# Kernel optimization log

Measured on AMD Instinct MI355X. Metric: run time of the kernel, lower is better.

## Reference

```python
import jax, jax.numpy as jnp
import numpy as np

N, E, G = 200000, 1200000, 2048
NODE_DIM, H = 5, 64
NEG_SLOPE = 0.2


def setup_inputs() -> dict:
    key = jax.random.key(0)
    ks = jax.random.split(key, 20)
    def glorot(k, shape):
        fan = sum(shape) if len(shape) > 1 else shape[0] + 1
        return jax.random.normal(k, shape, jnp.float32) * jnp.sqrt(2.0 / fan)
    inp = {
        'x': jax.random.normal(ks[0], (N, NODE_DIM), jnp.float32),
        'edge_index': jax.random.randint(ks[1], (2, E), 0, N, jnp.int64),
        'batch': jnp.sort(jax.random.randint(ks[2], (N,), 0, G, jnp.int64)),
        'embed_W': glorot(ks[3], (NODE_DIM, H)), 'embed_b': jnp.zeros((H,), jnp.float32),
        'g1_W': glorot(ks[4], (H, H)), 'g1_asrc': glorot(ks[5], (H,)), 'g1_adst': glorot(ks[6], (H,)), 'g1_b': jnp.zeros((H,), jnp.float32),
        'g2_W': glorot(ks[7], (H, H)), 'g2_asrc': glorot(ks[8], (H,)), 'g2_adst': glorot(ks[9], (H,)), 'g2_b': jnp.zeros((H,), jnp.float32),
        'fc1_W': glorot(ks[10], (2 * H, 64)), 'fc1_b': jnp.zeros((64,), jnp.float32),
        'fc2_W': glorot(ks[11], (64, 32)), 'fc2_b': jnp.zeros((32,), jnp.float32),
        'fc3_W': glorot(ks[12], (32, 1)), 'fc3_b': jnp.zeros((1,), jnp.float32),
    }
    return inp


def gat_conv(x, src, dst, W, a_src, a_dst, b):
    # x: [N, H] -> h: [N, H]; edges (with self-loops) src->dst
    h = x @ W
    alpha_s = h @ a_src  # [N]
    alpha_d = h @ a_dst  # [N]
    e = jax.nn.leaky_relu(alpha_s[src] + alpha_d[dst], NEG_SLOPE)  # [E']
    m = jax.ops.segment_max(e, dst, num_segments=N)
    w = jnp.exp(e - m[dst])
    denom = jax.ops.segment_sum(w, dst, num_segments=N)
    alpha = w / (denom[dst] + 1e-16)
    out = jax.ops.segment_sum(h[src] * alpha[:, None], dst, num_segments=N)
    return out + b


def reference(x, edge_index, batch, embed_W, embed_b,
              g1_W, g1_asrc, g1_adst, g1_b,
              g2_W, g2_asrc, g2_adst, g2_b,
              fc1_W, fc1_b, fc2_W, fc2_b, fc3_W, fc3_b):
    # add self loops once (PyG GATConv default add_self_loops=True)
    loops = jnp.arange(N, dtype=edge_index.dtype)
    src = jnp.concatenate([edge_index[0], loops])
    dst = jnp.concatenate([edge_index[1], loops])

    h = x @ embed_W + embed_b
    h = gat_conv(h, src, dst, g1_W, g1_asrc, g1_adst, g1_b)
    h = jax.nn.relu(h)
    h = gat_conv(h, src, dst, g2_W, g2_asrc, g2_adst, g2_b)

    # global mean / max pooling per graph
    cnt = jax.ops.segment_sum(jnp.ones((N,), h.dtype), batch, num_segments=G)
    mean = jax.ops.segment_sum(h, batch, num_segments=G) / jnp.maximum(cnt, 1.0)[:, None]
    mx = jax.ops.segment_max(h, batch, num_segments=G)
    mx = jnp.where(cnt[:, None] > 0, mx, 0.0)
    g = jnp.concatenate([mean, mx], axis=1)  # [G, 2H]

    g = jax.nn.relu(g @ fc1_W + fc1_b)
    g = jax.nn.relu(g @ fc2_W + fc2_b)
    return g @ fc3_W + fc3_b  # [G, 1]
```

## Files before the change

kernel.cpp:

```cpp
#include <hip/hip_runtime.h>
#include <hip/hip_bf16.h>
#include <hip/hip_fp16.h>

#define HD 64
#define NODE_DIM 5
#define NEG_SLOPE 0.2f
#define GT 64
#define BSH 9
#define BNODES 512
#define NBMAX 512
#define BCAP 4096
#define EPB 8
#define LDH 72

typedef _Float16 f16x8 __attribute__((ext_vector_type(8)));
typedef float f32x4 __attribute__((ext_vector_type(4)));

template <bool EMBED>
__global__ __launch_bounds__(256) void gemm_alpha_k(
    const void* __restrict__ hin, const float* __restrict__ embW,
    const float* __restrict__ embB, const float* __restrict__ W,
    const float* __restrict__ asrc, const float* __restrict__ adst,
    __half* __restrict__ hout, float* __restrict__ alpha_s,
    float* __restrict__ alpha_d, int N) {
    __shared__ _Float16 hs[GT * LDH];
    __shared__ _Float16 Wt[HD * LDH];
    __shared__ float xe[GT * NODE_DIM];
    __shared__ float we[NODE_DIM * HD + HD];
    const int t = threadIdx.x;
    const int n0 = blockIdx.x * GT;
    if (n0 >= N) return;
    const int rem = N - n0;

#pragma unroll
    for (int j = 0; j < 16; j++) {
        int idx = t + 256 * j;
        int k = idx >> 6, n = idx & 63;
        Wt[n * LDH + k] = (_Float16)W[idx];
    }

    if (EMBED) {
        const float* xin = (const float*)hin;
        for (int j = t; j < GT * NODE_DIM; j += 256)
            xe[j] = (j < rem * NODE_DIM) ? xin[(size_t)n0 * NODE_DIM + j] : 0.0f;
        for (int j = t; j < NODE_DIM * HD + HD; j += 256)
            we[j] = (j < NODE_DIM * HD) ? embW[j] : embB[j - NODE_DIM * HD];
        __syncthreads();
        int r = t >> 2, d0 = (t & 3) * 16;
#pragma unroll
        for (int jj = 0; jj < 16; jj++) {
            int d = d0 + jj;
            float acc = we[NODE_DIM * HD + d];
#pragma unroll
            for (int k = 0; k < NODE_DIM; k++)
                acc = fmaf(xe[r * NODE_DIM + k], we[k * HD + d], acc);
            hs[r * LDH + d] = (r < rem) ? (_Float16)acc : (_Float16)0.0f;
        }
    } else {
        const short4* g4 = (const short4*)((const __half*)hin + (size_t)n0 * HD);
#pragma unroll
        for (int j = 0; j < 4; j++) {
            int idx = t + 256 * j;
            int row = idx >> 4, c4 = idx & 15;
            short4 v = {0, 0, 0, 0};
            if (row < rem) v = g4[idx];
            *(short4*)(hs + row * LDH + c4 * 4) = v;
        }
    }
    __syncthreads();

    const int lane = t & 63;
    const int w = t >> 6;
    const int r16 = lane & 15;
    const int g = lane >> 4;

    const _Float16* hrow = hs + (w * 16 + r16) * LDH + g * 8;
    f16x8 b0 = *(const f16x8*)(hrow);
    f16x8 b1 = *(const f16x8*)(hrow + 32);

    f32x4 acc[4];
#pragma unroll
    for (int mt = 0; mt < 4; mt++) acc[mt] = (f32x4){0.f, 0.f, 0.f, 0.f};

#pragma unroll
    for (int mt = 0; mt < 4; mt++) {
        const _Float16* arow = Wt + (mt * 16 + r16) * LDH + g * 8;
        f16x8 a0 = *(const f16x8*)(arow);
        f16x8 a1 = *(const f16x8*)(arow + 32);
        acc[mt] = __builtin_amdgcn_mfma_f32_16x16x32_f16(a0, b0, acc[mt], 0, 0, 0);
        acc[mt] = __builtin_amdgcn_mfma_f32_16x16x32_f16(a1, b1, acc[mt], 0, 0, 0);
    }

    const int node = n0 + w * 16 + r16;
    float ps = 0.0f, pd = 0.0f;
    if (node < N) {
#pragma unroll
        for (int mt = 0; mt < 4; mt++) {
            float4 av = ((const float4*)asrc)[mt * 4 + g];
            float4 bv = ((const float4*)adst)[mt * 4 + g];
            ps += acc[mt][0] * av.x + acc[mt][1] * av.y +
                  acc[mt][2] * av.z + acc[mt][3] * av.w;
            pd += acc[mt][0] * bv.x + acc[mt][1] * bv.y +
                  acc[mt][2] * bv.z + acc[mt][3] * bv.w;
            short4 s;
            s.x = __half_as_short(__float2half_rn(acc[mt][0]));
            s.y = __half_as_short(__float2half_rn(acc[mt][1]));
            s.z = __half_as_short(__float2half_rn(acc[mt][2]));
            s.w = __half_as_short(__float2half_rn(acc[mt][3]));
            ((short4*)hout)[(size_t)node * 16 + mt * 4 + g] = s;
        }
    }
    ps += __shfl_xor(ps, 16);
    ps += __shfl_xor(ps, 32);
    pd += __shfl_xor(pd, 16);
    pd += __shfl_xor(pd, 32);
    if (g == 0 && node < N) {
        alpha_s[node] = ps;
        alpha_d[node] = pd;
    }
}


__global__ void zero_k(int* __restrict__ p, int total) {
    int i = blockIdx.x * blockDim.x + threadIdx.x;
    if (i < total) p[i] = 0;
}

__global__ __launch_bounds__(256) void partition_k(
    const int* __restrict__ ei, int* __restrict__ bcnt,
    int* __restrict__ bpack, int E) {
    __shared__ int lcnt[NBMAX], lbase[NBMAX];
    int dst[EPB], src[EPB];
    int jb = blockIdx.x * (256 * EPB) + threadIdx.x;
#pragma unroll
    for (int u = 0; u < EPB; u++) {
        int j = jb + u * 256;
        if (j < E) {
            dst[u] = __builtin_nontemporal_load(&ei[E + j]);
            src[u] = __builtin_nontemporal_load(&ei[j]);
        } else dst[u] = -1;
    }
    for (int b = threadIdx.x; b < NBMAX; b += 256) lcnt[b] = 0;
    __syncthreads();
#pragma unroll
    for (int u = 0; u < EPB; u++)
        if (dst[u] >= 0) atomicAdd(&lcnt[dst[u] >> BSH], 1);
    __syncthreads();
    for (int b = threadIdx.x; b < NBMAX; b += 256) {
        int c = lcnt[b];
        lbase[b] = c ? (b * BCAP + atomicAdd(&bcnt[b], c)) : 0;
        lcnt[b] = 0;
    }
    __syncthreads();
#pragma unroll
    for (int u = 0; u < EPB; u++) {
        if (dst[u] >= 0) {
            int b = dst[u] >> BSH;
            int o = atomicAdd(&lcnt[b], 1);
            bpack[lbase[b] + o] = (src[u] << BSH) | (dst[u] & (BNODES - 1));
        }
    }
}

__global__ void bucket_scan_k(const int* __restrict__ bcnt,
                              int* __restrict__ bbase, int NB) {
    __shared__ int s[NBMAX];
    int t = threadIdx.x;
    int v = (t < NB) ? bcnt[t] : 0;
    s[t] = v;
    __syncthreads();
#pragma unroll
    for (int o = 1; o < NBMAX; o <<= 1) {
        int tv = (t >= o) ? s[t - o] : 0;
        __syncthreads();
        s[t] += tv;
        __syncthreads();
    }
    if (t < NB) {
        bbase[t] = s[t] - v;
        if (t == NB - 1) bbase[NB] = s[t];
    }
}

__global__ __launch_bounds__(256) void bucket_csr_k(
    const int* __restrict__ bpack, const int* __restrict__ bcnt,
    const int* __restrict__ bbase,
    int* __restrict__ off, int* __restrict__ csr_src, int N) {
    __shared__ int s[BNODES];
    __shared__ int lcur[BNODES];
    const int t = threadIdx.x;
    const int b = blockIdx.x;
    const int nbase = b << BSH;
    const int cnt = bcnt[b];
    const int w0 = b * BCAP;
    const int e0 = bbase[b];

    s[t] = 0; s[t + 256] = 0;
    __syncthreads();
    for (int j = t; j < cnt; j += 256)
        atomicAdd(&s[bpack[w0 + j] & (BNODES - 1)], 1);
    __syncthreads();
    int d0 = s[t], d1 = s[t + 256];
#pragma unroll
    for (int o = 1; o < BNODES; o <<= 1) {
        int a0 = (t >= o) ? s[t - o] : 0;
        int a1 = (t + 256 >= o) ? s[t + 256 - o] : 0;
        __syncthreads();
        s[t] += a0;
        s[t + 256] += a1;
        __syncthreads();
    }
    int ex0 = s[t] - d0, ex1 = s[t + 256] - d1;
    lcur[t] = ex0; lcur[t + 256] = ex1;
    int n0 = nbase + t, n1 = nbase + t + 256;
    if (n0 < N) off[n0] = e0 + ex0;
    if (n1 < N) off[n1] = e0 + ex1;
    if (t == 255 && b == gridDim.x - 1) off[N] = e0 + cnt;
    __syncthreads();
    for (int j = t; j < cnt; j += 256) {
        int v = bpack[w0 + j];
        int pos = atomicAdd(&lcur[v & (BNODES - 1)], 1);
        csr_src[e0 + pos] = v >> BSH;
    }
}

template <bool BR>
__global__ __launch_bounds__(256) void gather_k(
    const int* __restrict__ off, const int* __restrict__ csr_src,
    const float* __restrict__ as, const float* __restrict__ ad,
    const __half* __restrict__ h, const float* __restrict__ bias,
    __half* __restrict__ out, int N) {
    int tid = blockIdx.x * blockDim.x + threadIdx.x;
    int wv = tid >> 6;
    int lane = threadIdx.x & 63;
    int grp = lane >> 4;
    int l16 = lane & 15;
    int n = wv * 4 + grp;
    if (n >= N) return;
    int s0 = off[n], s1 = off[n + 1];
    float adv = ad[n];
    const short4* h4 = (const short4*)h;

    float e = as[n] + adv;
    e = (e >= 0.0f) ? e : NEG_SLOPE * e;
    float wsl = __expf(e);
    float l0 = wsl, l1 = 0.0f;
    short4 hvs = h4[(unsigned)(n * 16 + l16)];
    float4 acc0, acc1 = {0, 0, 0, 0};
    acc0.x = wsl * __half2float(__short_as_half(hvs.x));
    acc0.y = wsl * __half2float(__short_as_half(hvs.y));
    acc0.z = wsl * __half2float(__short_as_half(hvs.z));
    acc0.w = wsl * __half2float(__short_as_half(hvs.w));

    int i = s0;
    for (; i + 4 <= s1; i += 4) {
        int src0 = csr_src[i], src1 = csr_src[i + 1];
        int src2 = csr_src[i + 2], src3 = csr_src[i + 3];
        float e0 = as[src0] + adv, e1 = as[src1] + adv;
        float e2 = as[src2] + adv, e3 = as[src3] + adv;
        short4 hv0 = h4[(unsigned)(src0 * 16 + l16)];
        short4 hv1 = h4[(unsigned)(src1 * 16 + l16)];
        short4 hv2 = h4[(unsigned)(src2 * 16 + l16)];
        short4 hv3 = h4[(unsigned)(src3 * 16 + l16)];
        e0 = (e0 >= 0.0f) ? e0 : NEG_SLOPE * e0;
        e1 = (e1 >= 0.0f) ? e1 : NEG_SLOPE * e1;
        e2 = (e2 >= 0.0f) ? e2 : NEG_SLOPE * e2;
        e3 = (e3 >= 0.0f) ? e3 : NEG_SLOPE * e3;
        float w0 = __expf(e0), w1 = __expf(e1), w2 = __expf(e2), w3 = __expf(e3);
        l0 += w0 + w2; l1 += w1 + w3;
        acc0.x = fmaf(w0, __half2float(__short_as_half(hv0.x)), acc0.x);
        acc0.y = fmaf(w0, __half2float(__short_as_half(hv0.y)), acc0.y);
        acc0.z = fmaf(w0, __half2float(__short_as_half(hv0.z)), acc0.z);
        acc0.w = fmaf(w0, __half2float(__short_as_half(hv0.w)), acc0.w);
        acc1.x = fmaf(w1, __half2float(__short_as_half(hv1.x)), acc1.x);
        acc1.y = fmaf(w1, __half2float(__short_as_half(hv1.y)), acc1.y);
        acc1.z = fmaf(w1, __half2float(__short_as_half(hv1.z)), acc1.z);
        acc1.w = fmaf(w1, __half2float(__short_as_half(hv1.w)), acc1.w);
        acc0.x = fmaf(w2, __half2float(__short_as_half(hv2.x)), acc0.x);
        acc0.y = fmaf(w2, __half2float(__short_as_half(hv2.y)), acc0.y);
        acc0.z = fmaf(w2, __half2float(__short_as_half(hv2.z)), acc0.z);
        acc0.w = fmaf(w2, __half2float(__short_as_half(hv2.w)), acc0.w);
        acc1.x = fmaf(w3, __half2float(__short_as_half(hv3.x)), acc1.x);
        acc1.y = fmaf(w3, __half2float(__short_as_half(hv3.y)), acc1.y);
        acc1.z = fmaf(w3, __half2float(__short_as_half(hv3.z)), acc1.z);
        acc1.w = fmaf(w3, __half2float(__short_as_half(hv3.w)), acc1.w);
    }
    for (; i + 2 <= s1; i += 2) {
        int src0 = csr_src[i], src1 = csr_src[i + 1];
        float e0 = as[src0] + adv;
        float e1 = as[src1] + adv;
        short4 hv0 = h4[(unsigned)(src0 * 16 + l16)];
        short4 hv1 = h4[(unsigned)(src1 * 16 + l16)];
        e0 = (e0 >= 0.0f) ? e0 : NEG_SLOPE * e0;
        e1 = (e1 >= 0.0f) ? e1 : NEG_SLOPE * e1;
        float w0 = __expf(e0), w1 = __expf(e1);
        l0 += w0; l1 += w1;
        acc0.x = fmaf(w0, __half2float(__short_as_half(hv0.x)), acc0.x);
        acc0.y = fmaf(w0, __half2float(__short_as_half(hv0.y)), acc0.y);
        acc0.z = fmaf(w0, __half2float(__short_as_half(hv0.z)), acc0.z);
        acc0.w = fmaf(w0, __half2float(__short_as_half(hv0.w)), acc0.w);
        acc1.x = fmaf(w1, __half2float(__short_as_half(hv1.x)), acc1.x);
        acc1.y = fmaf(w1, __half2float(__short_as_half(hv1.y)), acc1.y);
        acc1.z = fmaf(w1, __half2float(__short_as_half(hv1.z)), acc1.z);
        acc1.w = fmaf(w1, __half2float(__short_as_half(hv1.w)), acc1.w);
    }
    if (i < s1) {
        int src0 = csr_src[i];
        float e0 = as[src0] + adv;
        short4 hv0 = h4[(unsigned)(src0 * 16 + l16)];
        e0 = (e0 >= 0.0f) ? e0 : NEG_SLOPE * e0;
        float w0 = __expf(e0);
        l0 += w0;
        acc0.x = fmaf(w0, __half2float(__short_as_half(hv0.x)), acc0.x);
        acc0.y = fmaf(w0, __half2float(__short_as_half(hv0.y)), acc0.y);
        acc0.z = fmaf(w0, __half2float(__short_as_half(hv0.z)), acc0.z);
        acc0.w = fmaf(w0, __half2float(__short_as_half(hv0.w)), acc0.w);
    }
    float inv = 1.0f / (l0 + l1 + 1e-16f);
    float4 r;
    r.x = (acc0.x + acc1.x) * inv;
    r.y = (acc0.y + acc1.y) * inv;
    r.z = (acc0.z + acc1.z) * inv;
    r.w = (acc0.w + acc1.w) * inv;
    if (BR) {
        float4 b = ((const float4*)bias)[l16];
        r.x = fmaxf(r.x + b.x, 0.0f);
        r.y = fmaxf(r.y + b.y, 0.0f);
        r.z = fmaxf(r.z + b.z, 0.0f);
        r.w = fmaxf(r.w + b.w, 0.0f);
    }
    short4 o;
    o.x = __half_as_short(__float2half_rn(r.x));
    o.y = __half_as_short(__float2half_rn(r.y));
    o.z = __half_as_short(__float2half_rn(r.z));
    o.w = __half_as_short(__float2half_rn(r.w));
    ((short4*)out)[(unsigned)(n * 16 + l16)] = o;
}

__global__ __launch_bounds__(256) void pool_mlp_k(
    const __half* __restrict__ hfin, const float* __restrict__ hb,
    const int* __restrict__ batch, int N,
    const float* __restrict__ fc1W, const float* __restrict__ fc1b,
    const float* __restrict__ fc2W, const float* __restrict__ fc2b,
    const float* __restrict__ fc3W, const float* __restrict__ fc3b,
    float* __restrict__ out) {
    __shared__ float psum[4][64];
    __shared__ float pmax[4][64];
    __shared__ float lds[192];
    int g = blockIdx.x;
    int lane = threadIdx.x & 63;
    int w = threadIdx.x >> 6;
    int lo = 0, hi = N;
    while (lo < hi) { int mid = (lo + hi) >> 1; if (batch[mid] < g) lo = mid + 1; else hi = mid; }
    int start = lo;
    lo = start; hi = N;
    while (lo < hi) { int mid = (lo + hi) >> 1; if (batch[mid] < g + 1) lo = mid + 1; else hi = mid; }
    int end = lo;
    float bias = hb[lane];
    float sum = 0.0f, mx = -INFINITY;
    for (int n = start + w; n < end; n += 4) {
        float v = __half2float(hfin[(size_t)n * HD + lane]) + bias;
        sum += v;
        mx = fmaxf(mx, v);
    }
    psum[w][lane] = sum;
    pmax[w][lane] = mx;
    __syncthreads();
    if (w == 0) {
        int cnt = end - start;
        float s = psum[0][lane] + psum[1][lane] + psum[2][lane] + psum[3][lane];
        float m = fmaxf(fmaxf(pmax[0][lane], pmax[1][lane]),
                        fmaxf(pmax[2][lane], pmax[3][lane]));
        lds[lane] = (cnt > 0) ? s / (float)cnt : 0.0f;
        lds[64 + lane] = (cnt > 0) ? m : 0.0f;
    }
    __syncthreads();
    if (w == 0) {
        float o1 = fc1b[lane];
        for (int k = 0; k < 128; k++) o1 += lds[k] * fc1W[k * 64 + lane];
        o1 = fmaxf(o1, 0.0f);
        __builtin_amdgcn_s_barrier();
        lds[128 + lane] = o1;
        float o2 = 0.0f;
        if (lane < 32) {
            o2 = fc2b[lane];
            for (int k = 0; k < 64; k++) o2 += lds[128 + k] * fc2W[k * 32 + lane];
            o2 = fmaxf(o2, 0.0f);
        }
        float part = (lane < 32) ? o2 * fc3W[lane] : 0.0f;
#pragma unroll
        for (int off = 32; off; off >>= 1) part += __shfl_xor(part, off);
        if (lane == 0) out[g] = part + fc3b[0];
    }
}

static inline size_t align256(size_t x) { return (x + 255) & ~(size_t)255; }

extern "C" void kernel_launch(void* const* d_in, const int* in_sizes, int n_in,
                              void* d_out, int out_size, void* d_ws, size_t ws_size,
                              hipStream_t stream) {
    const float* x      = (const float*)d_in[0];
    const int*   ei     = (const int*)d_in[1];
    const int*   batch  = (const int*)d_in[2];
    const float* embW   = (const float*)d_in[3];
    const float* embB   = (const float*)d_in[4];
    const float* g1W    = (const float*)d_in[5];
    const float* g1as   = (const float*)d_in[6];
    const float* g1ad   = (const float*)d_in[7];
    const float* g1b    = (const float*)d_in[8];
    const float* g2W    = (const float*)d_in[9];
    const float* g2as   = (const float*)d_in[10];
    const float* g2ad   = (const float*)d_in[11];
    const float* g2b    = (const float*)d_in[12];
    const float* fc1W   = (const float*)d_in[13];
    const float* fc1b   = (const float*)d_in[14];
    const float* fc2W   = (const float*)d_in[15];
    const float* fc2b   = (const float*)d_in[16];
    const float* fc3W   = (const float*)d_in[17];
    const float* fc3b   = (const float*)d_in[18];
    float* out = (float*)d_out;

    const int N  = in_sizes[0] / NODE_DIM;
    const int E  = in_sizes[1] / 2;
    const int G  = out_size;
    const int NH = N * HD;
    const int NB = (N + BNODES - 1) >> BSH;

    char* ws = (char*)d_ws;
    __half* bufA    = (__half*)ws; ws += align256((size_t)NH * 2);
    __half* bufB    = (__half*)ws; ws += align256((size_t)NH * 2);
    float*  as_buf  = (float*)ws;  ws += align256((size_t)N * 4);
    float*  ad_buf  = (float*)ws;  ws += align256((size_t)N * 4);
    int*    off     = (int*)ws;    ws += align256((size_t)(N + 1) * 4);
    int*    bcnt    = (int*)ws;    ws += align256((size_t)NBMAX * 4);
    int*    bbase   = (int*)ws;    ws += align256((size_t)(NBMAX + 1) * 4);
    int*    bpack   = (int*)ws;    ws += align256((size_t)NB * BCAP * 4);
    int*    csrsrc  = (int*)ws;    ws += align256((size_t)E * 4);

    const int B = 256;
    dim3 blk(B);
    dim3 gr_gemm((N + GT - 1) / GT);
    dim3 gr_gath(((N + 3) / 4 * 64 + B - 1) / B);
    dim3 gr_epb((E + B * EPB - 1) / (B * EPB));
    dim3 gr_n((N + B - 1) / B);

    zero_k<<<dim3(2), blk, 0, stream>>>(bcnt, NBMAX);
    partition_k<<<gr_epb, blk, 0, stream>>>(ei, bcnt, bpack, E);
    bucket_scan_k<<<dim3(1), dim3(NBMAX), 0, stream>>>(bcnt, bbase, NB);
    bucket_csr_k<<<dim3(NB), blk, 0, stream>>>(bpack, bcnt, bbase, off, csrsrc, N);

    gemm_alpha_k<true><<<gr_gemm, blk, 0, stream>>>(x, embW, embB, g1W, g1as, g1ad,
                                                    bufB, as_buf, ad_buf, N);
    gather_k<true><<<gr_gath, blk, 0, stream>>>(off, csrsrc, as_buf, ad_buf,
                                                bufB, g1b, bufA, N);

    gemm_alpha_k<false><<<gr_gemm, blk, 0, stream>>>(bufA, nullptr, nullptr, g2W,
                                                     g2as, g2ad, bufB, as_buf, ad_buf, N);
    gather_k<false><<<gr_gath, blk, 0, stream>>>(off, csrsrc, as_buf, ad_buf,
                                                 bufB, nullptr, bufA, N);

    pool_mlp_k<<<dim3(G), dim3(256), 0, stream>>>(bufA, g2b, batch, N,
                                                  fc1W, fc1b, fc2W, fc2b, fc3W, fc3b, out);
}
```

Measured before the change: 277.7 us.

## Fold bucket zeroing and scan into other kernels, widen pooling loads

Removes the zero_k and bucket_scan_k launches. Bucket counters are now zeroed by block 0 of the embedding GEMM kernel, and each bucket_csr block computes its own exclusive prefix by summing the preceding bucket counts in shared memory. The pooling kernel now reads short4 vectors with 16 node groups per block instead of 64 scalar lanes across 4 waves, and adds the bias once after reduction. This saves two kernel launches and gives pooling more memory parallelism. In exchange, every CSR block repeats the prefix reduction.

```diff
diff --git a/kernel.cpp b/kernel.cpp
--- a/kernel.cpp
+++ b/kernel.cpp
@@ -22,13 +22,16 @@
     const float* __restrict__ embB, const float* __restrict__ W,
     const float* __restrict__ asrc, const float* __restrict__ adst,
     __half* __restrict__ hout, float* __restrict__ alpha_s,
-    float* __restrict__ alpha_d, int N) {
+    float* __restrict__ alpha_d, int* __restrict__ bcnt0, int N) {
     __shared__ _Float16 hs[GT * LDH];
     __shared__ _Float16 Wt[HD * LDH];
     __shared__ float xe[GT * NODE_DIM];
     __shared__ float we[NODE_DIM * HD + HD];
     const int t = threadIdx.x;
     const int n0 = blockIdx.x * GT;
+    if (EMBED && blockIdx.x == 0) {
+        for (int j = t; j < NBMAX; j += 256) bcnt0[j] = 0;
+    }
     if (n0 >= N) return;
     const int rem = N - n0;
 
@@ -121,11 +124,6 @@
 }
 
 
-__global__ void zero_k(int* __restrict__ p, int total) {
-    int i = blockIdx.x * blockDim.x + threadIdx.x;
-    if (i < total) p[i] = 0;
-}
-
 __global__ __launch_bounds__(256) void partition_k(
     const int* __restrict__ ei, int* __restrict__ bcnt,
     int* __restrict__ bpack, int E) {
@@ -162,41 +160,30 @@
     }
 }
 
-__global__ void bucket_scan_k(const int* __restrict__ bcnt,
-                              int* __restrict__ bbase, int NB) {
-    __shared__ int s[NBMAX];
-    int t = threadIdx.x;
-    int v = (t < NB) ? bcnt[t] : 0;
-    s[t] = v;
-    __syncthreads();
-#pragma unroll
-    for (int o = 1; o < NBMAX; o <<= 1) {
-        int tv = (t >= o) ? s[t - o] : 0;
-        __syncthreads();
-        s[t] += tv;
-        __syncthreads();
-    }
-    if (t < NB) {
-        bbase[t] = s[t] - v;
-        if (t == NB - 1) bbase[NB] = s[t];
-    }
-}
-
 __global__ __launch_bounds__(256) void bucket_csr_k(
     const int* __restrict__ bpack, const int* __restrict__ bcnt,
-    const int* __restrict__ bbase,
-    int* __restrict__ off, int* __restrict__ csr_src, int N) {
+    int* __restrict__ off, int* __restrict__ csr_src, int N, int NB) {
     __shared__ int s[BNODES];
     __shared__ int lcur[BNODES];
+    __shared__ int sred[256];
     const int t = threadIdx.x;
     const int b = blockIdx.x;
     const int nbase = b << BSH;
     const int cnt = bcnt[b];
     const int w0 = b * BCAP;
-    const int e0 = bbase[b];
-
+
+    int part = 0;
+    for (int j = t; j < b; j += 256) part += bcnt[j];
+    sred[t] = part;
     s[t] = 0; s[t + 256] = 0;
     __syncthreads();
+#pragma unroll
+    for (int o = 128; o; o >>= 1) {
+        if (t < o) sred[t] += sred[t + o];
+        __syncthreads();
+    }
+    const int e0 = sred[0];
+
     for (int j = t; j < cnt; j += 256)
         atomicAdd(&s[bpack[w0 + j] & (BNODES - 1)], 1);
     __syncthreads();
@@ -215,7 +202,7 @@
     int n0 = nbase + t, n1 = nbase + t + 256;
     if (n0 < N) off[n0] = e0 + ex0;
     if (n1 < N) off[n1] = e0 + ex1;
-    if (t == 255 && b == gridDim.x - 1) off[N] = e0 + cnt;
+    if (t == 0 && b == NB - 1) off[N] = e0 + cnt;
     __syncthreads();
     for (int j = t; j < cnt; j += 256) {
         int v = bpack[w0 + j];
@@ -344,38 +331,50 @@
     const float* __restrict__ fc2W, const float* __restrict__ fc2b,
     const float* __restrict__ fc3W, const float* __restrict__ fc3b,
     float* __restrict__ out) {
-    __shared__ float psum[4][64];
-    __shared__ float pmax[4][64];
+    __shared__ float psum[16][64];
+    __shared__ float pmax[16][64];
     __shared__ float lds[192];
     int g = blockIdx.x;
-    int lane = threadIdx.x & 63;
-    int w = threadIdx.x >> 6;
+    int t = threadIdx.x;
+    int gg = t >> 4;
+    int l16 = t & 15;
     int lo = 0, hi = N;
     while (lo < hi) { int mid = (lo + hi) >> 1; if (batch[mid] < g) lo = mid + 1; else hi = mid; }
     int start = lo;
     lo = start; hi = N;
     while (lo < hi) { int mid = (lo + hi) >> 1; if (batch[mid] < g + 1) lo = mid + 1; else hi = mid; }
     int end = lo;
-    float bias = hb[lane];
-    float sum = 0.0f, mx = -INFINITY;
-    for (int n = start + w; n < end; n += 4) {
-        float v = __half2float(hfin[(size_t)n * HD + lane]) + bias;
-        sum += v;
-        mx = fmaxf(mx, v);
-    }
-    psum[w][lane] = sum;
-    pmax[w][lane] = mx;
-    __syncthreads();
-    if (w == 0) {
+    const short4* h4 = (const short4*)hfin;
+    float4 sum = {0, 0, 0, 0};
+    float4 mx = {-INFINITY, -INFINITY, -INFINITY, -INFINITY};
+    for (int n = start + gg; n < end; n += 16) {
+        short4 v = h4[(size_t)n * 16 + l16];
+        float a = __half2float(__short_as_half(v.x));
+        float b = __half2float(__short_as_half(v.y));
+        float c = __half2float(__short_as_half(v.z));
+        float d = __half2float(__short_as_half(v.w));
+        sum.x += a; sum.y += b; sum.z += c; sum.w += d;
+        mx.x = fmaxf(mx.x, a); mx.y = fmaxf(mx.y, b);
+        mx.z = fmaxf(mx.z, c); mx.w = fmaxf(mx.w, d);
+    }
+    *(float4*)&psum[gg][l16 * 4] = sum;
+    *(float4*)&pmax[gg][l16 * 4] = mx;
+    __syncthreads();
+    if (t < 64) {
+        float s = 0.0f, m = -INFINITY;
+#pragma unroll
+        for (int k = 0; k < 16; k++) {
+            s += psum[k][t];
+            m = fmaxf(m, pmax[k][t]);
+        }
         int cnt = end - start;
-        float s = psum[0][lane] + psum[1][lane] + psum[2][lane] + psum[3][lane];
-        float m = fmaxf(fmaxf(pmax[0][lane], pmax[1][lane]),
-                        fmaxf(pmax[2][lane], pmax[3][lane]));
-        lds[lane] = (cnt > 0) ? s / (float)cnt : 0.0f;
-        lds[64 + lane] = (cnt > 0) ? m : 0.0f;
-    }
-    __syncthreads();
-    if (w == 0) {
+        float bias = hb[t];
+        lds[t]      = (cnt > 0) ? s / (float)cnt + bias : 0.0f;
+        lds[64 + t] = (cnt > 0) ? m + bias : 0.0f;
+    }
+    __syncthreads();
+    if (t < 64) {
+        int lane = t;
         float o1 = fc1b[lane];
         for (int k = 0; k < 128; k++) o1 += lds[k] * fc1W[k * 64 + lane];
         o1 = fmaxf(o1, 0.0f);
@@ -433,7 +432,6 @@
     float*  ad_buf  = (float*)ws;  ws += align256((size_t)N * 4);
     int*    off     = (int*)ws;    ws += align256((size_t)(N + 1) * 4);
     int*    bcnt    = (int*)ws;    ws += align256((size_t)NBMAX * 4);
-    int*    bbase   = (int*)ws;    ws += align256((size_t)(NBMAX + 1) * 4);
     int*    bpack   = (int*)ws;    ws += align256((size_t)NB * BCAP * 4);
     int*    csrsrc  = (int*)ws;    ws += align256((size_t)E * 4);
 
@@ -442,20 +440,18 @@
     dim3 gr_gemm((N + GT - 1) / GT);
     dim3 gr_gath(((N + 3) / 4 * 64 + B - 1) / B);
     dim3 gr_epb((E + B * EPB - 1) / (B * EPB));
-    dim3 gr_n((N + B - 1) / B);
-
-    zero_k<<<dim3(2), blk, 0, stream>>>(bcnt, NBMAX);
+
+    gemm_alpha_k<true><<<gr_gemm, blk, 0, stream>>>(x, embW, embB, g1W, g1as, g1ad,
+                                                    bufB, as_buf, ad_buf, bcnt, N);
     partition_k<<<gr_epb, blk, 0, stream>>>(ei, bcnt, bpack, E);
-    bucket_scan_k<<<dim3(1), dim3(NBMAX), 0, stream>>>(bcnt, bbase, NB);
-    bucket_csr_k<<<dim3(NB), blk, 0, stream>>>(bpack, bcnt, bbase, off, csrsrc, N);
-
-    gemm_alpha_k<true><<<gr_gemm, blk, 0, stream>>>(x, embW, embB, g1W, g1as, g1ad,
-                                                    bufB, as_buf, ad_buf, N);
+    bucket_csr_k<<<dim3(NB), blk, 0, stream>>>(bpack, bcnt, off, csrsrc, N, NB);
+
     gather_k<true><<<gr_gath, blk, 0, stream>>>(off, csrsrc, as_buf, ad_buf,
                                                 bufB, g1b, bufA, N);
 
     gemm_alpha_k<false><<<gr_gemm, blk, 0, stream>>>(bufA, nullptr, nullptr, g2W,
-                                                     g2as, g2ad, bufB, as_buf, ad_buf, N);
+                                                     g2as, g2ad, bufB, as_buf, ad_buf,
+                                                     nullptr, N);
     gather_k<false><<<gr_gath, blk, 0, stream>>>(off, csrsrc, as_buf, ad_buf,
                                                  bufB, nullptr, bufA, N);
 
```

After: 265.0 us. 1.05x faster.
